# Kernel optimization log

Hardware: AMD Instinct MI355X
Metric: run time of the kernel (lower is better)

## Reference

```python
import jax, jax.numpy as jnp
import numpy as np

# Model constants (from module __init__ / repo script)
DT = 60                    # model time step [s]
DT_FORCING = 3600          # forcing time step [s]
NSUB = DT_FORCING // DT    # substeps between forcing samples = 60
NT = 5_040_000             # number of model steps (~9.6 years at dt=60s)
NF = NT // NSUB            # forcing series length = 84000
FC = 1e-4                  # Coriolis frequency


def setup_inputs() -> dict:
    key = jax.random.key(0)
    k1, k2, k3 = jax.random.split(key, 3)
    # pk = log(K); K ~ exp(-10) ~ 4.5e-5 keeps the Euler recurrence stable (|a|<1)
    pk = -10.0 + 0.1 * jax.random.normal(k1, (2,), dtype=jnp.float32)
    # wind stress forcing, around the repo's 0.2 N/m^2 zonal value
    TAx = 0.2 + 0.05 * jax.random.normal(k2, (NF,), dtype=jnp.float32)
    TAy = 0.05 * jax.random.normal(k3, (NF,), dtype=jnp.float32)
    return {"pk": pk, "TAx": TAx, "TAy": TAy}


def reference(pk, TAx, TAy):
    K = jnp.exp(pk)                                    # K[0]: wind coeff, K[1]: damping
    TA = TAx.astype(jnp.complex64) + 1j * TAy.astype(jnp.complex64)  # [NF]

    # Vectorized linear interpolation of forcing onto every model step it=0..NT-2
    it = jnp.arange(NT - 1)
    itf = it // NSUB
    aa = (it % NSUB).astype(jnp.float32) / NSUB
    # faithful to original: compares against NT (never true), then relies on
    # JAX's clamping gather for the final out-of-range itf+1
    itsup = jnp.where(itf + 1 >= NT, -1, itf + 1)
    TAi = (1.0 - aa) * TA[itf] + aa * TA[itsup]        # [NT-1] complex64

    # U_{t+1} = U_t + dt*(-i*fc*U_t + K0*TA_t - K1*U_t) = a*U_t + b_t
    a = jnp.asarray(1.0 + DT * (-1j * FC - K[1]), dtype=jnp.complex64)
    b = (DT * K[0]).astype(jnp.complex64) * TAi        # [NT-1]

    def step(u, bt):
        u_next = a * u + bt
        return u_next, u_next

    u0 = jnp.zeros((), dtype=jnp.complex64)
    _, ys = jax.lax.scan(step, u0, b)                  # [NT-1]
    U = jnp.concatenate([u0[None], ys])                # [NT], U[0] = 0
    return jnp.real(U), jnp.imag(U)
```

## Files before the change

kernel.cpp:

```cpp
#include <hip/hip_runtime.h>
#include <math.h>

#define NTOT   5040000
#define NFORC  84000
#define NSTEPS (NTOT - 1)

#define TPB    256
#define SEGS   60
#define WIN    (TPB * SEGS)
#define WARM   4800
#define CHUNK  (WIN - WARM)
#define NBLK   ((NSTEPS + CHUNK - 1) / CHUNK)

struct cd { double x, y; };
__device__ __forceinline__ cd cmuld(cd a, cd b){ return {a.x*b.x - a.y*b.y, a.x*b.y + a.y*b.x}; }
__device__ __forceinline__ cd cdivd(cd a, cd b){
    double r = 1.0 / (b.x*b.x + b.y*b.y);
    return {(a.x*b.x + a.y*b.y)*r, (a.y*b.x - a.x*b.y)*r};
}

__device__ __forceinline__ float2 cfma(float2 m, float2 p, float2 v) {
    v.x = fmaf(m.x, p.x, fmaf(-m.y, p.y, v.x));
    v.y = fmaf(m.x, p.y, fmaf( m.y, p.x, v.y));
    return v;
}
__device__ __forceinline__ float2 cmulf(float2 a, float2 b){
    return make_float2(a.x*b.x - a.y*b.y, a.x*b.y + a.y*b.x);
}

__global__ __launch_bounds__(TPB, 4)
void slab_kernel(const float* __restrict__ pk,
                 const float* __restrict__ TAx,
                 const float* __restrict__ TAy,
                 float* __restrict__ out)
{
    __shared__ float2 wk[4];

    const int tid  = threadIdx.x;
    const int lane = tid & 63;
    const int wv   = tid >> 6;
    const int blk  = blockIdx.x;

    const double K0 = exp((double)pk[0]);
    const double K1 = exp((double)pk[1]);
    const cd a   = {1.0 - 60.0 * K1, -60.0e-4};
    const double s = 60.0 * K0;

    cd alpha = {1.0, 0.0};
    {
        cd p = a; int e = SEGS;
        while (e) { if (e & 1) alpha = cmuld(alpha, p); p = cmuld(p, p); e >>= 1; }
    }
    const cd am1 = {a.x - 1.0, a.y};
    const cd G = cdivd({alpha.x - 1.0, alpha.y}, am1);
    const cd a59 = cdivd(alpha, a);
    const cd one_m_a = {-am1.x, -am1.y};
    cd num = {1.0 - 60.0*a59.x + 59.0*alpha.x, -60.0*a59.y + 59.0*alpha.y};
    const cd T = cdivd(cmuld(a, num), cmuld(one_m_a, one_m_a));
    const cd H = {59.0*G.x - T.x, 59.0*G.y - T.y};

    const float2 Gf = make_float2((float)G.x, (float)G.y);
    const float2 Hf = make_float2((float)H.x, (float)H.y);
    float2 apf[6];
    float2 betaf;
    {
        cd p = alpha;
        #pragma unroll
        for (int k = 0; k < 6; ++k) { apf[k] = make_float2((float)p.x, (float)p.y); p = cmuld(p, p); }
        betaf = make_float2((float)p.x, (float)p.y);
    }
    const float ar  = (float)a.x;
    const float aii = (float)a.y;

    const int wstart = blk * CHUNK;
    const int wend   = min(wstart + CHUNK, NSTEPS);
    const int ws     = max(0, wstart - WARM);
    const int seg    = ws + tid * SEGS;

    const int itf = ws / SEGS + tid;
    const int i0  = min(itf,     NFORC - 1);
    const int i1  = min(itf + 1, NFORC - 1);
    const float x0 = TAx[i0], y0 = TAy[i0];
    const float x1 = TAx[i1], y1 = TAy[i1];
    const float sF = (float)s;
    const float2 b0 = make_float2(sF * x0, sF * y0);
    const float  ci = sF * (1.0f / 60.0f);
    const float2 db = make_float2((x1 - x0) * ci, (y1 - y0) * ci);

    float2 S = cfma(Gf, b0, cmulf(Hf, db));

    #pragma unroll
    for (int k = 0; k < 6; ++k) {
        const int off = 1 << k;
        float px = __shfl_up(S.x, off, 64);
        float py = __shfl_up(S.y, off, 64);
        if (lane < off) { px = 0.f; py = 0.f; }
        S = cfma(apf[k], make_float2(px, py), S);
    }
    float ex = __shfl_up(S.x, 1, 64);
    float ey = __shfl_up(S.y, 1, 64);
    if (lane == 0) { ex = 0.f; ey = 0.f; }

    if (lane == 63) wk[wv] = S;
    __syncthreads();
    float2 C = make_float2(0.f, 0.f);
    if (wv >= 1) C = wk[0];
    if (wv >= 2) C = cfma(betaf, C, wk[1]);
    if (wv == 3) C = cfma(betaf, C, wk[2]);

    float2 al = make_float2(1.f, 0.f);
    #pragma unroll
    for (int k = 0; k < 6; ++k)
        if (lane & (1 << k)) al = cmulf(al, apf[k]);

    float2 u0 = cfma(al, C, make_float2(ex, ey));

    if (blk == 0 && tid == 0) { out[0] = 0.f; out[NTOT] = 0.f; }

    const bool live = (seg >= wstart);
    const int  nv   = wend - seg;
    if (!live || nv <= 0) return;

    float ur = u0.x, ui = u0.y;
    float bre = b0.x, bim = b0.y;
    const float dbx = db.x, dby = db.y;
    float* __restrict__ pr = out + (seg + 1);
    float* __restrict__ pi = out + (NTOT + seg + 1);

#define STEP() do { \
        float nr_ = fmaf(ar, ur, fmaf(-aii, ui, bre)); \
        float ni_ = fmaf(ar, ui, fmaf( aii, ur, bim)); \
        ur = nr_; ui = ni_; bre += dbx; bim += dby; } while (0)

    if (nv >= SEGS) {
        #pragma unroll
        for (int k = 0; k < 3; ++k) { STEP(); pr[k] = ur; pi[k] = ui; }
        #pragma unroll
        for (int g = 0; g < 14; ++g) {
            float4 vr, vi;
            STEP(); vr.x = ur; vi.x = ui;
            STEP(); vr.y = ur; vi.y = ui;
            STEP(); vr.z = ur; vi.z = ui;
            STEP(); vr.w = ur; vi.w = ui;
            *reinterpret_cast<float4*>(pr + 3 + 4*g) = vr;
            *reinterpret_cast<float4*>(pi + 3 + 4*g) = vi;
        }
        STEP(); pr[59] = ur; pi[59] = ui;
    } else {
        for (int k = 0; k < SEGS; ++k) {
            STEP();
            if (k < nv) { pr[k] = ur; pi[k] = ui; }
        }
    }
#undef STEP
}

extern "C" void kernel_launch(void* const* d_in, const int* in_sizes, int n_in,
                              void* d_out, int out_size, void* d_ws, size_t ws_size,
                              hipStream_t stream)
{
    const float* pk  = (const float*)d_in[0];
    const float* TAx = (const float*)d_in[1];
    const float* TAy = (const float*)d_in[2];
    float* out = (float*)d_out;

    slab_kernel<<<dim3(NBLK), dim3(TPB), 0, stream>>>(pk, TAx, TAy, out);
}
```

Baseline: 88.89 us.

## Evaluate outputs in closed form per step from shared segment states

Replaces the per-thread sequential 60-step recurrence in the output phase with a direct closed-form evaluation. Every output element is computed as a^r*u0 + G_r*b0 + H_r*db, with the per-offset coefficient tables and per-segment states held in shared memory. All threads of the block now share the output work, and the stores become coalesced float4 writes across threads instead of each thread writing a strided 60-element run. The cost is extra shared memory, an added barrier, 60 threads computing double-precision powers and divisions, and an integer divide plus shared-memory loads for each output.

```diff
diff --git a/kernel.cpp b/kernel.cpp
--- a/kernel.cpp
+++ b/kernel.cpp
@@ -18,6 +18,11 @@
     double r = 1.0 / (b.x*b.x + b.y*b.y);
     return {(a.x*b.x + a.y*b.y)*r, (a.y*b.x - a.x*b.y)*r};
 }
+__device__ __forceinline__ cd cpowd(cd a, int e){
+    cd r = {1.0, 0.0}; cd p = a;
+    while (e) { if (e & 1) r = cmuld(r, p); p = cmuld(p, p); e >>= 1; }
+    return r;
+}
 
 __device__ __forceinline__ float2 cfma(float2 m, float2 p, float2 v) {
     v.x = fmaf(m.x, p.x, fmaf(-m.y, p.y, v.x));
@@ -34,6 +39,8 @@
                  const float* __restrict__ TAy,
                  float* __restrict__ out)
 {
+    __shared__ float2 sA[SEGS], sG[SEGS], sH[SEGS];
+    __shared__ float2 sU0[TPB], sB0[TPB], sDB[TPB];
     __shared__ float2 wk[4];
 
     const int tid  = threadIdx.x;
@@ -45,37 +52,44 @@
     const double K1 = exp((double)pk[1]);
     const cd a   = {1.0 - 60.0 * K1, -60.0e-4};
     const double s = 60.0 * K0;
+    const cd am1     = {a.x - 1.0, a.y};
+    const cd one_m_a = {-am1.x, -am1.y};
+    const cd om2     = cmuld(one_m_a, one_m_a);
 
-    cd alpha = {1.0, 0.0};
-    {
-        cd p = a; int e = SEGS;
-        while (e) { if (e & 1) alpha = cmuld(alpha, p); p = cmuld(p, p); e >>= 1; }
-    }
-    const cd am1 = {a.x - 1.0, a.y};
-    const cd G = cdivd({alpha.x - 1.0, alpha.y}, am1);
+    const cd alpha = cpowd(a, SEGS);
+    const cd G60 = cdivd({alpha.x - 1.0, alpha.y}, am1);
     const cd a59 = cdivd(alpha, a);
-    const cd one_m_a = {-am1.x, -am1.y};
-    cd num = {1.0 - 60.0*a59.x + 59.0*alpha.x, -60.0*a59.y + 59.0*alpha.y};
-    const cd T = cdivd(cmuld(a, num), cmuld(one_m_a, one_m_a));
-    const cd H = {59.0*G.x - T.x, 59.0*G.y - T.y};
+    cd num60 = {1.0 - 60.0*a59.x + 59.0*alpha.x, -60.0*a59.y + 59.0*alpha.y};
+    const cd T60 = cdivd(cmuld(a, num60), om2);
+    const cd H60 = {59.0*G60.x - T60.x, 59.0*G60.y - T60.y};
 
-    const float2 Gf = make_float2((float)G.x, (float)G.y);
-    const float2 Hf = make_float2((float)H.x, (float)H.y);
-    float2 apf[6];
-    float2 betaf;
+    const float2 Gf = make_float2((float)G60.x, (float)G60.y);
+    const float2 Hf = make_float2((float)H60.x, (float)H60.y);
+    float2 apf[6]; float2 betaf;
     {
         cd p = alpha;
         #pragma unroll
         for (int k = 0; k < 6; ++k) { apf[k] = make_float2((float)p.x, (float)p.y); p = cmuld(p, p); }
         betaf = make_float2((float)p.x, (float)p.y);
     }
-    const float ar  = (float)a.x;
-    const float aii = (float)a.y;
+
+    if (tid < SEGS) {
+        const int j = tid + 1;
+        const cd aj = cpowd(a, j);
+        const cd Gj = cdivd({aj.x - 1.0, aj.y}, am1);
+        const cd ajm1 = cdivd(aj, a);
+        cd nm = {1.0 - (double)j*ajm1.x + (double)(j-1)*aj.x,
+                      - (double)j*ajm1.y + (double)(j-1)*aj.y};
+        const cd Tj = cdivd(cmuld(a, nm), om2);
+        const cd Hj = {(double)(j-1)*Gj.x - Tj.x, (double)(j-1)*Gj.y - Tj.y};
+        sA[tid] = make_float2((float)aj.x, (float)aj.y);
+        sG[tid] = make_float2((float)Gj.x, (float)Gj.y);
+        sH[tid] = make_float2((float)Hj.x, (float)Hj.y);
+    }
 
     const int wstart = blk * CHUNK;
     const int wend   = min(wstart + CHUNK, NSTEPS);
     const int ws     = max(0, wstart - WARM);
-    const int seg    = ws + tid * SEGS;
 
     const int itf = ws / SEGS + tid;
     const int i0  = min(itf,     NFORC - 1);
@@ -86,6 +100,8 @@
     const float2 b0 = make_float2(sF * x0, sF * y0);
     const float  ci = sF * (1.0f / 60.0f);
     const float2 db = make_float2((x1 - x0) * ci, (y1 - y0) * ci);
+    sB0[tid] = b0;
+    sDB[tid] = db;
 
     float2 S = cfma(Gf, b0, cmulf(Hf, db));
 
@@ -113,46 +129,46 @@
     for (int k = 0; k < 6; ++k)
         if (lane & (1 << k)) al = cmulf(al, apf[k]);
 
-    float2 u0 = cfma(al, C, make_float2(ex, ey));
+    const float2 u0 = cfma(al, C, make_float2(ex, ey));
+    sU0[tid] = u0;
+    __syncthreads();
 
     if (blk == 0 && tid == 0) { out[0] = 0.f; out[NTOT] = 0.f; }
 
-    const bool live = (seg >= wstart);
-    const int  nv   = wend - seg;
-    if (!live || nv <= 0) return;
+    const int qlo = wstart + 1;
+    const int qhi = wend + 1;
+    const int g0  = qlo & ~3;
+    const int ng  = (qhi - g0 + 3) >> 2;
 
-    float ur = u0.x, ui = u0.y;
-    float bre = b0.x, bim = b0.y;
-    const float dbx = db.x, dby = db.y;
-    float* __restrict__ pr = out + (seg + 1);
-    float* __restrict__ pi = out + (NTOT + seg + 1);
-
-#define STEP() do { \
-        float nr_ = fmaf(ar, ur, fmaf(-aii, ui, bre)); \
-        float ni_ = fmaf(ar, ui, fmaf( aii, ur, bim)); \
-        ur = nr_; ui = ni_; bre += dbx; bim += dby; } while (0)
-
-    if (nv >= SEGS) {
+    for (int k = tid; k < ng; k += TPB) {
+        const int q4 = g0 + (k << 2);
+        float re[4], im[4];
         #pragma unroll
-        for (int k = 0; k < 3; ++k) { STEP(); pr[k] = ur; pi[k] = ui; }
-        #pragma unroll
-        for (int g = 0; g < 14; ++g) {
-            float4 vr, vi;
-            STEP(); vr.x = ur; vi.x = ui;
-            STEP(); vr.y = ur; vi.y = ui;
-            STEP(); vr.z = ur; vi.z = ui;
-            STEP(); vr.w = ur; vi.w = ui;
-            *reinterpret_cast<float4*>(pr + 3 + 4*g) = vr;
-            *reinterpret_cast<float4*>(pi + 3 + 4*g) = vi;
+        for (int e = 0; e < 4; ++e) {
+            const int q = q4 + e;
+            if (q < qlo || q >= qhi) { re[e] = 0.f; im[e] = 0.f; continue; }
+            const int m   = q - 1 - ws;
+            const int seg = (int)((unsigned)m / 60u);
+            const int r   = m - seg * 60;
+            const float2 A  = sA[r];
+            const float2 Gv = sG[r];
+            const float2 Hv = sH[r];
+            float2 u = cmulf(A, sU0[seg]);
+            u = cfma(Gv, sB0[seg], u);
+            u = cfma(Hv, sDB[seg], u);
+            re[e] = u.x; im[e] = u.y;
         }
-        STEP(); pr[59] = ur; pi[59] = ui;
-    } else {
-        for (int k = 0; k < SEGS; ++k) {
-            STEP();
-            if (k < nv) { pr[k] = ur; pi[k] = ui; }
+        if (q4 >= qlo && q4 + 4 <= qhi) {
+            *reinterpret_cast<float4*>(out + q4)        = make_float4(re[0], re[1], re[2], re[3]);
+            *reinterpret_cast<float4*>(out + NTOT + q4) = make_float4(im[0], im[1], im[2], im[3]);
+        } else {
+            #pragma unroll
+            for (int e = 0; e < 4; ++e) {
+                const int q = q4 + e;
+                if (q >= qlo && q < qhi) { out[q] = re[e]; out[NTOT + q] = im[e]; }
+            }
         }
     }
-#undef STEP
 }
 
 extern "C" void kernel_launch(void* const* d_in, const int* in_sizes, int n_in,
```

After: 80.80 us. 9.1% less time.
